# Kernel tuning notes

Measured on AMD Instinct MI355X. Metric: run time of the kernel, lower is better.

Reference implementation:

```python
import jax, jax.numpy as jnp
import numpy as np

BIG = 1e10  # sentinel distance used by the original code


def _index_points(points, idx):
    # points: [B,N,C], idx: [B,N,8] -> [B,N,8,C]
    return jax.vmap(lambda p, i: p[i])(points, idx)


def _pointsift_select(radius, xyz):
    """Octant-wise nearest neighbor within radius. xyz: [B,N,3] -> idx int32 [B,N,8]."""
    B, N, _ = xyz.shape
    judge = radius ** 2
    # diff[b,n,p] = xyz[b,p] - xyz[b,n]
    diff = xyz[:, None, :, :] - xyz[:, :, None, :]            # [B,N,N,3]
    dist = jnp.sum(diff * diff, axis=-1)                      # [B,N,N]
    # octant code: ((p - n) + 1) truncated to int, dotted with [4,2,1]
    octw = jnp.array([4, 2, 1], dtype=jnp.int32)
    code = jnp.sum((diff + 1.0).astype(jnp.int32) * octw, axis=-1)  # [B,N,N]
    diag = jnp.eye(N, dtype=bool)[None]                       # self entry -> judge_dist
    idx_per_oct = []
    for i in range(8):
        d = jnp.where((code == i) & (dist > 1e-10) & (dist < judge), dist, BIG)
        d = jnp.where(diag, judge, d)
        idx_per_oct.append(jnp.argmin(d, axis=-1))            # first-min, matches torch.min
    return jnp.stack(idx_per_oct, axis=-1).astype(jnp.int32)  # [B,N,8]


def setup_inputs() -> dict:
    key = jax.random.key(0)
    k1, k2 = jax.random.split(key)
    B, N, C = 2, 4096, 64
    xyz = jax.random.uniform(k1, (B, N, 3), dtype=jnp.float32)
    points = jax.random.normal(k2, (B, N, C), dtype=jnp.float32)
    return {"xyz": xyz, "points": points, "radius": 0.25}


def reference(xyz, points, radius):
    B, N, _ = xyz.shape
    idx = _pointsift_select(radius, xyz)                      # [B,N,8]
    grouped_xyz = _index_points(xyz, idx) - xyz[:, :, None, :]  # [B,N,8,3]
    grouped_feats = _index_points(points, idx)                # [B,N,8,C]
    grouped_points = jnp.concatenate([grouped_xyz, grouped_feats], axis=-1)  # use_xyz=True
    return grouped_xyz, grouped_points, idx
```

## Files before the change

### kernel.cpp

```cpp
#include <hip/hip_runtime.h>

#define BB 2
#define NN 4096
#define CC 64
#define QPB 4
#define TPQ 64
#define NT 256

#define OUT0_OFF 0
#define OUT1_OFF (BB * NN * 8 * 3)
#define OUT2_OFF (OUT1_OFF + BB * NN * 8 * 67)

#define WS_SORTED_BYTES (BB * NN * 16)

__global__ __launch_bounds__(1024) void build_grid(
    const float* __restrict__ xyz, float4* __restrict__ sorted,
    int* __restrict__ offsets)
{
    __shared__ int hist[64];
    __shared__ int offs[65];
    const int b = blockIdx.x;
    const int tid = threadIdx.x;
    if (tid < 64) hist[tid] = 0;
    __syncthreads();
    const float* src = xyz + (size_t)b * NN * 3;
    #pragma unroll
    for (int p = tid; p < NN; p += 1024) {
        float x = src[p * 3 + 0], y = src[p * 3 + 1], z = src[p * 3 + 2];
        int cell = (((int)(x * 4.0f)) << 4) | (((int)(y * 4.0f)) << 2)
                 | ((int)(z * 4.0f));
        atomicAdd(&hist[cell], 1);
    }
    __syncthreads();
    if (tid < 64) {
        int inc = hist[tid];
        #pragma unroll
        for (int d = 1; d < 64; d <<= 1) {
            int u = __shfl_up(inc, d, 64);
            if (tid >= d) inc += u;
        }
        offs[tid + 1] = inc;
        if (tid == 0) offs[0] = 0;
    }
    __syncthreads();
    if (tid < 65) offsets[b * 65 + tid] = offs[tid];
    if (tid < 64) hist[tid] = offs[tid];
    __syncthreads();
    float4* dst = sorted + (size_t)b * NN;
    #pragma unroll
    for (int p = tid; p < NN; p += 1024) {
        float x = src[p * 3 + 0], y = src[p * 3 + 1], z = src[p * 3 + 2];
        int cell = (((int)(x * 4.0f)) << 4) | (((int)(y * 4.0f)) << 2)
                 | ((int)(z * 4.0f));
        int pos = atomicAdd(&hist[cell], 1);
        dst[pos] = make_float4(x, y, z, __uint_as_float((unsigned)p));
    }
}

__global__ __launch_bounds__(NT, 8) void pointsift_select(
    const float4* __restrict__ sorted, const int* __restrict__ offsets,
    const float* __restrict__ radius_p, float* __restrict__ out)
{
    __shared__ int s_off[65];

    const int tid = threadIdx.x;
    const int blk = blockIdx.x;
    const int b = blk >> 10;
    const int qslot = (blk & 1023) * QPB;
    const float4* sb = sorted + (size_t)b * NN;

    if (tid < 65) s_off[tid] = offsets[b * 65 + tid];

    const float r = radius_p[0];
    const float judge = __fmul_rn(r, r);
    const unsigned OFFC = __float_as_uint(1e-10f) + 1u;
    const unsigned seedkey = __float_as_uint(judge) - OFFC;

    const int g = tid >> 6;
    const float4 q = sb[qslot + g];
    const unsigned n = __float_as_uint(q.w);
    const float qx = q.x, qy = q.y, qz = q.z;
    const int sub = tid & 63;

    unsigned long long bv[8];
    const unsigned long long seed64 = ((unsigned long long)seedkey << 32) | n;
    #pragma unroll
    for (int o = 0; o < 8; ++o) bv[o] = seed64;

    const int lx = max(0, (int)((qx - r) * 4.0f));
    const int hx = min(3, (int)((qx + r) * 4.0f));
    const int ly = max(0, (int)((qy - r) * 4.0f));
    const int hy = min(3, (int)((qy + r) * 4.0f));
    const int lz = max(0, (int)((qz - r) * 4.0f));
    const int hz = min(3, (int)((qz + r) * 4.0f));

    __syncthreads();

    for (int cx = lx; cx <= hx; ++cx) {
        for (int cy = ly; cy <= hy; ++cy) {
            const int cb = (cx << 4) | (cy << 2);
            const int s = s_off[cb + lz];
            const int e = s_off[cb + hz + 1];
            #pragma unroll 2
            for (int p = s + sub; p < e; p += TPQ) {
                float4 c = sb[p];
                float dx = __fsub_rn(c.x, qx);
                float dy = __fsub_rn(c.y, qy);
                float dz = __fsub_rn(c.z, qz);
                float dist = __fadd_rn(__fadd_rn(__fmul_rn(dx, dx),
                                                 __fmul_rn(dy, dy)),
                                       __fmul_rn(dz, dz));
                unsigned ikey = __float_as_uint(dist) - OFFC;
                ikey = (dist >= judge) ? 0xFFFFFFFFu : ikey;
                int code = (((int)__fadd_rn(dx, 1.0f)) * 4 +
                            ((int)__fadd_rn(dy, 1.0f)) * 2 +
                            ((int)__fadd_rn(dz, 1.0f)));
                unsigned long long key64 =
                    ((unsigned long long)ikey << 32) |
                    (unsigned long long)__float_as_uint(c.w);
                #pragma unroll
                for (int o = 0; o < 8; ++o) {
                    unsigned long long cand =
                        (code == o) ? key64 : 0xFFFFFFFFFFFFFFFFull;
                    bv[o] = (cand < bv[o]) ? cand : bv[o];
                }
            }
        }
    }

    #pragma unroll
    for (int mm = 1; mm < TPQ; mm <<= 1) {
        #pragma unroll
        for (int o = 0; o < 8; ++o) {
            unsigned long long ov = __shfl_xor(bv[o], mm, 64);
            if (ov < bv[o]) bv[o] = ov;
        }
    }

    if (sub == 0) {
        const size_t tb = ((size_t)b * NN + n) * 8;
        #pragma unroll
        for (int o = 0; o < 8; ++o)
            out[OUT2_OFF + tb + o] = (float)(unsigned)(bv[o] & 0xFFFFFFFFu);
    }
}

#define GT_TPW 8
__global__ __launch_bounds__(256, 8) void pointsift_gather(
    const float* __restrict__ xyz, const float* __restrict__ points,
    float* __restrict__ out)
{
    const int tid = threadIdx.x;
    const int wave = tid >> 6;
    const int lane = tid & 63;
    const int base_t = (blockIdx.x * 4 + wave) * GT_TPW;

    int idxs[GT_TPW];
    #pragma unroll
    for (int k = 0; k < GT_TPW; ++k)
        idxs[k] = (int)out[OUT2_OFF + base_t + k];

    #pragma unroll
    for (int k = 0; k < GT_TPW; ++k) {
        const int t = base_t + k;
        const int i = idxs[k];
        const int bn = t >> 3;
        const int b = bn >> 12;
        const int n = bn & (NN - 1);
        const float* xb = xyz + (size_t)b * NN * 3;
        const float* pb = points + (size_t)b * NN * CC;
        float v;
        if (lane < 3) v = __fsub_rn(xb[i * 3 + lane], xb[n * 3 + lane]);
        else          v = pb[(size_t)i * CC + (lane - 3)];
        out[OUT1_OFF + (size_t)t * 67 + lane] = v;
        if (lane >= 61)
            out[OUT1_OFF + (size_t)t * 67 + (lane + 3)] = pb[(size_t)i * CC + lane];
        if (lane < 3)
            out[OUT0_OFF + (size_t)t * 3 + lane] = v;
    }
}

extern "C" void kernel_launch(void* const* d_in, const int* in_sizes, int n_in,
                              void* d_out, int out_size, void* d_ws, size_t ws_size,
                              hipStream_t stream) {
    const float* xyz    = (const float*)d_in[0];
    const float* points = (const float*)d_in[1];
    const float* radius = (const float*)d_in[2];
    float* out = (float*)d_out;
    float4* ws_sorted = (float4*)d_ws;
    int* ws_offsets = (int*)((char*)d_ws + WS_SORTED_BYTES);

    hipLaunchKernelGGL(build_grid, dim3(BB), dim3(1024), 0, stream,
                       xyz, ws_sorted, ws_offsets);
    hipLaunchKernelGGL(pointsift_select,
                       dim3(BB * (NN / QPB)), dim3(NT), 0, stream,
                       ws_sorted, ws_offsets, radius, out);
    hipLaunchKernelGGL(pointsift_gather,
                       dim3(BB * NN * 8 / (4 * GT_TPW)), dim3(256), 0, stream,
                       xyz, points, out);
}
```

Baseline: 103.2 us.

## Fuse neighbor gather into select kernel and use nontemporal stores

Merges the separate gather kernel into the octant-select kernel. After the butterfly reduction every lane of the query's wave holds all eight neighbor indices, so each lane writes one output channel directly. This removes a kernel launch and the round trip of the indices through global memory. The gathered outputs are written with nontemporal stores. The risk is that the gather now runs inside a heavier kernel, and the dynamic register-array index for the idx write may be lowered inefficiently.

```diff
diff --git a/kernel.cpp b/kernel.cpp
--- a/kernel.cpp
+++ b/kernel.cpp
@@ -57,8 +57,9 @@
     }
 }
 
-__global__ __launch_bounds__(NT, 8) void pointsift_select(
+__global__ __launch_bounds__(NT, 8) void select_gather(
     const float4* __restrict__ sorted, const int* __restrict__ offsets,
+    const float* __restrict__ xyz, const float* __restrict__ points,
     const float* __restrict__ radius_p, float* __restrict__ out)
 {
     __shared__ int s_off[65];
@@ -137,46 +138,26 @@
         }
     }
 
-    if (sub == 0) {
-        const size_t tb = ((size_t)b * NN + n) * 8;
-        #pragma unroll
-        for (int o = 0; o < 8; ++o)
-            out[OUT2_OFF + tb + o] = (float)(unsigned)(bv[o] & 0xFFFFFFFFu);
-    }
-}
+    const size_t tb = ((size_t)b * NN + n) * 8;
+    if (sub < 8)
+        out[OUT2_OFF + tb + sub] = (float)(unsigned)(bv[sub] & 0xFFFFFFFFu);
 
-#define GT_TPW 8
-__global__ __launch_bounds__(256, 8) void pointsift_gather(
-    const float* __restrict__ xyz, const float* __restrict__ points,
-    float* __restrict__ out)
-{
-    const int tid = threadIdx.x;
-    const int wave = tid >> 6;
-    const int lane = tid & 63;
-    const int base_t = (blockIdx.x * 4 + wave) * GT_TPW;
-
-    int idxs[GT_TPW];
+    const float* xb = xyz + (size_t)b * NN * 3;
+    const float* pb = points + (size_t)b * NN * CC;
+    const float qc = (sub == 0) ? qx : ((sub == 1) ? qy : qz);
     #pragma unroll
-    for (int k = 0; k < GT_TPW; ++k)
-        idxs[k] = (int)out[OUT2_OFF + base_t + k];
-
-    #pragma unroll
-    for (int k = 0; k < GT_TPW; ++k) {
-        const int t = base_t + k;
-        const int i = idxs[k];
-        const int bn = t >> 3;
-        const int b = bn >> 12;
-        const int n = bn & (NN - 1);
-        const float* xb = xyz + (size_t)b * NN * 3;
-        const float* pb = points + (size_t)b * NN * CC;
+    for (int o = 0; o < 8; ++o) {
+        const int i = (int)(unsigned)(bv[o] & 0xFFFFFFFFu);
+        const size_t t = tb + o;
         float v;
-        if (lane < 3) v = __fsub_rn(xb[i * 3 + lane], xb[n * 3 + lane]);
-        else          v = pb[(size_t)i * CC + (lane - 3)];
-        out[OUT1_OFF + (size_t)t * 67 + lane] = v;
-        if (lane >= 61)
-            out[OUT1_OFF + (size_t)t * 67 + (lane + 3)] = pb[(size_t)i * CC + lane];
-        if (lane < 3)
-            out[OUT0_OFF + (size_t)t * 3 + lane] = v;
+        if (sub < 3) v = __fsub_rn(xb[i * 3 + sub], qc);
+        else         v = pb[(size_t)i * CC + (sub - 3)];
+        __builtin_nontemporal_store(v, &out[OUT1_OFF + t * 67 + sub]);
+        if (sub >= 61)
+            __builtin_nontemporal_store(pb[(size_t)i * CC + sub],
+                                        &out[OUT1_OFF + t * 67 + (sub + 3)]);
+        if (sub < 3)
+            __builtin_nontemporal_store(v, &out[OUT0_OFF + t * 3 + sub]);
     }
 }
 
@@ -192,10 +173,7 @@
 
     hipLaunchKernelGGL(build_grid, dim3(BB), dim3(1024), 0, stream,
                        xyz, ws_sorted, ws_offsets);
-    hipLaunchKernelGGL(pointsift_select,
+    hipLaunchKernelGGL(select_gather,
                        dim3(BB * (NN / QPB)), dim3(NT), 0, stream,
-                       ws_sorted, ws_offsets, radius, out);
-    hipLaunchKernelGGL(pointsift_gather,
-                       dim3(BB * NN * 8 / (4 * GT_TPW)), dim3(256), 0, stream,
-                       xyz, points, out);
+                       ws_sorted, ws_offsets, xyz, points, radius, out);
 }
```

New measurement: 102.6 us. Within noise of the previous version (-0.6%).
